# Kernel optimization log

Measured on AMD Instinct MI355X. Metric: run time of the kernel, lower is better.

The kernel has to match this reference:

```python
import jax, jax.numpy as jnp
import numpy as np

K = 3

def setup_inputs() -> dict:
    key = jax.random.key(0)
    k1, k2, k3, k4 = jax.random.split(key, 4)
    B, N, F_in, T, F_out = 8, 2048, 16, 12, 32
    x = jax.random.normal(k1, (B, N, F_in, T), dtype=jnp.float32)
    spatial_attention = jax.random.uniform(k2, (B, N, N), dtype=jnp.float32)
    node_embeddings = jax.random.normal(k3, (N, 16), dtype=jnp.float32)
    theta = jax.random.normal(k4, (K, F_in, F_out), dtype=jnp.float32) * 0.1
    return {"x": x, "spatial_attention": spatial_attention,
            "node_embeddings": node_embeddings, "theta": theta}

def _cheb_polys(node_embeddings, N, K):
    # supports = softmax(relu(E E^T), axis=1)
    supports = jax.nn.softmax(jax.nn.relu(node_embeddings @ node_embeddings.T), axis=1)
    polys = [jnp.eye(N, dtype=supports.dtype), supports]
    for _ in range(2, K):
        polys.append(2.0 * supports @ polys[-1] - polys[-2])
    return jnp.stack(polys[:K], axis=0)  # (K, N, N)

def reference(x, spatial_attention, node_embeddings, theta):
    B, N, F_in, T = x.shape
    polys = _cheb_polys(node_embeddings, N, K)             # (K,N,N)
    # T_k_with_at = polys[k] * attention (broadcast over batch);
    # rhs = T_k_with_at^T @ graph_signal for every timestep:
    # (K,N,N)*(B,N,N) contracted with (B,N,F,T) over source node n -> (K,B,M,F,T)
    rhs = jnp.einsum('knm,bnm,bnft->kbmft', polys, spatial_attention, x)
    # accumulate rhs @ theta_k over k -> (B,M,F_out,T)
    out = jnp.einsum('kbmft,kfo->bmot', rhs, theta)
    return jax.nn.relu(out)
```

## Files before the change

kernel.cpp:

```cpp
#include <hip/hip_runtime.h>

#define NN    2048
#define BATCH 8
#define FIN   16
#define TT    12
#define FOUT  32
#define FT    (FIN*TT)
#define OT    (FOUT*TT)

typedef unsigned short ushort_t;
typedef __attribute__((ext_vector_type(8))) short   short8;
typedef __attribute__((ext_vector_type(4))) float   f32x4;
typedef __attribute__((ext_vector_type(4))) unsigned short us4;
typedef __attribute__((ext_vector_type(8))) unsigned short us8;

__device__ __forceinline__ float b2f(unsigned short u) {
    union { unsigned int i; float f; } v; v.i = ((unsigned int)u) << 16; return v.f;
}
__device__ __forceinline__ unsigned short f2b(float f) {
    union { float f; unsigned int i; } v; v.f = f;
    unsigned int x = v.i;
    x += 0x7fffu + ((x >> 16) & 1u);
    return (unsigned short)(x >> 16);
}

__global__ __launch_bounds__(256)
void k_supports(const float* __restrict__ E, ushort_t* __restrict__ Sb) {
    const int n = blockIdx.x;
    __shared__ float row[NN];
    __shared__ float red[256];
    const int tid = threadIdx.x;

    float en[16];
    #pragma unroll
    for (int j = 0; j < 16; ++j) en[j] = E[n * 16 + j];

    float lmax = 0.0f;
    for (int m = tid; m < NN; m += 256) {
        float d = 0.0f;
        #pragma unroll
        for (int j = 0; j < 16; ++j) d += en[j] * E[m * 16 + j];
        d = fmaxf(d, 0.0f);
        row[m] = d;
        lmax = fmaxf(lmax, d);
    }
    red[tid] = lmax; __syncthreads();
    for (int s = 128; s > 0; s >>= 1) {
        if (tid < s) red[tid] = fmaxf(red[tid], red[tid + s]);
        __syncthreads();
    }
    const float mx = red[0];
    __syncthreads();

    float lsum = 0.0f;
    for (int m = tid; m < NN; m += 256) {
        float e = __expf(row[m] - mx);
        row[m] = e;
        lsum += e;
    }
    red[tid] = lsum; __syncthreads();
    for (int s = 128; s > 0; s >>= 1) {
        if (tid < s) red[tid] += red[tid + s];
        __syncthreads();
    }
    const float inv = 1.0f / red[0];
    for (int m = tid; m < NN; m += 256) Sb[(size_t)n * NN + m] = f2b(row[m] * inv);
}

__global__ __launch_bounds__(256)
void k_pack_st(const ushort_t* __restrict__ Sb, ushort_t* __restrict__ SbT) {
    const int r0 = blockIdx.x * 64, c0 = blockIdx.y * 64;
    __shared__ ushort_t Lt[64][65];
    const int tid = threadIdx.x;
    #pragma unroll
    for (int p = 0; p < 2; ++p) {
        const int i = (tid >> 3) + p * 32;
        const int j8 = (tid & 7) * 8;
        us8 v = *(const us8*)&Sb[(size_t)(r0 + i) * NN + c0 + j8];
        #pragma unroll
        for (int e = 0; e < 8; ++e) Lt[i][j8 + e] = v[e];
    }
    __syncthreads();
    #pragma unroll
    for (int p = 0; p < 2; ++p) {
        const int jj = (tid >> 3) + p * 32;
        const int i8 = (tid & 7) * 8;
        us8 v;
        #pragma unroll
        for (int e = 0; e < 8; ++e) v[e] = Lt[i8 + e][jj];
        *(us8*)&SbT[(size_t)(c0 + jj) * NN + r0 + i8] = v;
    }
}

__global__ __launch_bounds__(256)
void k_pack_x(const float* __restrict__ x, ushort_t* __restrict__ xbT) {
    const int nc = blockIdx.x * 64;
    const int b  = blockIdx.y;
    __shared__ ushort_t Lt[FT][65];
    const int tid = threadIdx.x;
    const float* __restrict__ xb = x + (size_t)b * NN * FT;
    #pragma unroll
    for (int p = 0; p < 12; ++p) {
        const int id = tid + 256 * p;
        const int nn = id / 48;
        const int f4 = (id % 48) * 4;
        const float4 v = *(const float4*)&xb[(size_t)(nc + nn) * FT + f4];
        Lt[f4 + 0][nn] = f2b(v.x);
        Lt[f4 + 1][nn] = f2b(v.y);
        Lt[f4 + 2][nn] = f2b(v.z);
        Lt[f4 + 3][nn] = f2b(v.w);
    }
    __syncthreads();
    #pragma unroll
    for (int p = 0; p < 6; ++p) {
        const int id = tid + 256 * p;
        const int ft = id >> 3;
        const int n8 = (id & 7) * 8;
        us8 v;
        #pragma unroll
        for (int e = 0; e < 8; ++e) v[e] = Lt[ft][n8 + e];
        *(us8*)&xbT[((size_t)b * FT + ft) * NN + nc + n8] = v;
    }
}

__global__ __launch_bounds__(256)
void k_t2(const ushort_t* __restrict__ Sb, const ushort_t* __restrict__ SbT,
          ushort_t* __restrict__ T2b) {
    const int m0 = blockIdx.x * 64;
    const int n0 = blockIdx.y * 64;
    __shared__ __align__(16) ushort_t As[2][64 * 64];
    __shared__ __align__(16) ushort_t Bs[2][64 * 64];
    const int tid = threadIdx.x;
    const int lane = tid & 63, w = tid >> 6;
    const int l15 = lane & 15, q = lane >> 4, l7 = lane & 7;
    const int n0w = (w & 1) * 32, m0w = (w >> 1) * 32;
    const int sr = tid >> 3;
    const int sc = tid & 7;

    f32x4 acc[2][2];
    #pragma unroll
    for (int i = 0; i < 2; ++i)
        #pragma unroll
        for (int j = 0; j < 2; ++j) acc[i][j] = {0.f, 0.f, 0.f, 0.f};

    us8 av[2], bv[2];
    #pragma unroll
    for (int p = 0; p < 2; ++p) {
        const int row = sr + 32 * p;
        av[p] = *(const us8*)&Sb[(size_t)(n0 + row) * NN + sc * 8];
        bv[p] = *(const us8*)&SbT[(size_t)(m0 + row) * NN + sc * 8];
    }
    #pragma unroll
    for (int p = 0; p < 2; ++p) {
        const int row = sr + 32 * p;
        const int cs = (sc ^ (row & 7)) * 8;
        *(us8*)&As[0][row * 64 + cs] = av[p];
        *(us8*)&Bs[0][row * 64 + cs] = bv[p];
    }
    for (int it = 0; it < 32; ++it) {
        __syncthreads();
        const int cur = it & 1;
        if (it < 31) {
            const int l0 = (it + 1) * 64;
            #pragma unroll
            for (int p = 0; p < 2; ++p) {
                const int row = sr + 32 * p;
                av[p] = *(const us8*)&Sb[(size_t)(n0 + row) * NN + l0 + sc * 8];
                bv[p] = *(const us8*)&SbT[(size_t)(m0 + row) * NN + l0 + sc * 8];
            }
        }
        #pragma unroll
        for (int s = 0; s < 2; ++s) {
            short8 a[2], bb[2];
            const int u = ((s * 4 + q) ^ l7) * 8;
            #pragma unroll
            for (int i = 0; i < 2; ++i)
                a[i] = *(const short8*)&As[cur][(n0w + i * 16 + l15) * 64 + u];
            #pragma unroll
            for (int j = 0; j < 2; ++j)
                bb[j] = *(const short8*)&Bs[cur][(m0w + j * 16 + l15) * 64 + u];
            #pragma unroll
            for (int i = 0; i < 2; ++i)
                #pragma unroll
                for (int j = 0; j < 2; ++j)
                    acc[i][j] = __builtin_amdgcn_mfma_f32_16x16x32_bf16(a[i], bb[j], acc[i][j], 0, 0, 0);
        }
        if (it < 31) {
            const int nxt = cur ^ 1;
            #pragma unroll
            for (int p = 0; p < 2; ++p) {
                const int row = sr + 32 * p;
                const int cs = (sc ^ (row & 7)) * 8;
                *(us8*)&As[nxt][row * 64 + cs] = av[p];
                *(us8*)&Bs[nxt][row * 64 + cs] = bv[p];
            }
        }
    }
    #pragma unroll
    for (int i = 0; i < 2; ++i)
        #pragma unroll
        for (int j = 0; j < 2; ++j)
            #pragma unroll
            for (int r = 0; r < 4; ++r) {
                const int ng = n0 + n0w + i * 16 + q * 4 + r;
                const int mg = m0 + m0w + j * 16 + l15;
                const float v = 2.0f * acc[i][j][r] - (ng == mg ? 1.0f : 0.0f);
                T2b[(size_t)ng * NN + mg] = f2b(v);
            }
}

__global__ __launch_bounds__(256)
void k_rhs(const ushort_t* __restrict__ Sb, const ushort_t* __restrict__ T2b,
           const float* __restrict__ att, const ushort_t* __restrict__ xbT,
           float* __restrict__ rhs) {
    const int m0 = blockIdx.x * 32;
    const int b  = blockIdx.y;
    __shared__ __align__(16) ushort_t As[2][2 * 32 * 64];
    __shared__ __align__(16) ushort_t Xs[2][FT * 64];
    const int tid = threadIdx.x;
    const int lane = tid & 63, w = tid >> 6;
    const int l15 = lane & 15, q = lane >> 4, l7 = lane & 7, l3 = lane >> 3;
    const int k1 = w & 1, ft0 = (w >> 1) * 96;
    const float* __restrict__ attb = att + (size_t)b * NN * NN;

    const int k1s = tid >> 7;
    const int uu  = tid & 127;
    const int m4  = (uu & 7) * 4;
    const int nn4 = (uu >> 3) * 4;
    const ushort_t* __restrict__ Pk = k1s ? T2b : Sb;

    f32x4 acc[2][6];
    #pragma unroll
    for (int i = 0; i < 2; ++i)
        #pragma unroll
        for (int t = 0; t < 6; ++t) acc[i][t] = {0.f, 0.f, 0.f, 0.f};

    us8   xv[6];
    us4   pv[4];
    f32x4 av4[4];

    #pragma unroll
    for (int p = 0; p < 6; ++p) {
        const int row = (w * 6 + p) * 8 + l3;
        xv[p] = *(const us8*)&xbT[((size_t)b * FT + row) * NN + l7 * 8];
    }
    #pragma unroll
    for (int r = 0; r < 4; ++r) {
        const int nn = nn4 + r;
        pv[r]  = *(const us4*)&Pk[(size_t)nn * NN + m0 + m4];
        av4[r] = *(const f32x4*)&attb[(size_t)nn * NN + m0 + m4];
    }
    #pragma unroll
    for (int p = 0; p < 6; ++p) {
        const int row = (w * 6 + p) * 8 + l3;
        *(us8*)&Xs[0][row * 64 + (l7 ^ l3) * 8] = xv[p];
    }
    #pragma unroll
    for (int c = 0; c < 4; ++c) {
        us4 wv;
        #pragma unroll
        for (int r = 0; r < 4; ++r) wv[r] = f2b(b2f(pv[r][c]) * av4[r][c]);
        const int rowm = m4 + c;
        const int off = (((nn4 >> 3) ^ (rowm & 7)) * 8) + (nn4 & 4);
        *(us4*)&As[0][(k1s * 32 + rowm) * 64 + off] = wv;
    }

    for (int it = 0; it < 32; ++it) {
        __syncthreads();
        const int cur = it & 1;
        if (it < 31) {
            const int nc = (it + 1) * 64;
            #pragma unroll
            for (int p = 0; p < 6; ++p) {
                const int row = (w * 6 + p) * 8 + l3;
                xv[p] = *(const us8*)&xbT[((size_t)b * FT + row) * NN + nc + l7 * 8];
            }
            #pragma unroll
            for (int r = 0; r < 4; ++r) {
                const int nn = nc + nn4 + r;
                pv[r]  = *(const us4*)&Pk[(size_t)nn * NN + m0 + m4];
                av4[r] = *(const f32x4*)&attb[(size_t)nn * NN + m0 + m4];
            }
        }
        #pragma unroll
        for (int s = 0; s < 2; ++s) {
            short8 a[2], bb[6];
            #pragma unroll
            for (int i = 0; i < 2; ++i) {
                const int row = i * 16 + l15;
                a[i] = *(const short8*)&As[cur][(k1 * 32 + row) * 64 + (((s * 4 + q) ^ l7) * 8)];
            }
            #pragma unroll
            for (int t = 0; t < 6; ++t) {
                const int col = ft0 + t * 16 + l15;
                const int u = ((s * 4 + q) ^ (col & 7)) * 8;
                bb[t] = *(const short8*)&Xs[cur][col * 64 + u];
            }
            #pragma unroll
            for (int i = 0; i < 2; ++i)
                #pragma unroll
                for (int t = 0; t < 6; ++t)
                    acc[i][t] = __builtin_amdgcn_mfma_f32_16x16x32_bf16(a[i], bb[t], acc[i][t], 0, 0, 0);
        }
        if (it < 31) {
            const int nxt = cur ^ 1;
            #pragma unroll
            for (int p = 0; p < 6; ++p) {
                const int row = (w * 6 + p) * 8 + l3;
                *(us8*)&Xs[nxt][row * 64 + (l7 ^ l3) * 8] = xv[p];
            }
            #pragma unroll
            for (int c = 0; c < 4; ++c) {
                us4 wv;
                #pragma unroll
                for (int r = 0; r < 4; ++r) wv[r] = f2b(b2f(pv[r][c]) * av4[r][c]);
                const int rowm = m4 + c;
                const int off = (((nn4 >> 3) ^ (rowm & 7)) * 8) + (nn4 & 4);
                *(us4*)&As[nxt][(k1s * 32 + rowm) * 64 + off] = wv;
            }
        }
    }
    float* __restrict__ op = rhs + ((size_t)(k1 * BATCH + b)) * NN * FT;
    #pragma unroll
    for (int i = 0; i < 2; ++i)
        #pragma unroll
        for (int t = 0; t < 6; ++t)
            #pragma unroll
            for (int r = 0; r < 4; ++r) {
                const int mg = m0 + i * 16 + q * 4 + r;
                const int ftg = ft0 + t * 16 + l15;
                op[(size_t)mg * FT + ftg] = acc[i][t][r];
            }
}

__global__ __launch_bounds__(128)
void k_out(const float* __restrict__ x, const float* __restrict__ att,
           const float* __restrict__ theta, const float* __restrict__ rhs,
           float* __restrict__ out) {
    const int m = blockIdx.x & (NN - 1);
    const int b = blockIdx.x >> 11;
    __shared__ float xr[FT], r1[FT], r2[FT];
    __shared__ float th[3 * FIN * FOUT];
    const int tid = threadIdx.x;

    const float* __restrict__ xb = x + ((size_t)b * NN + m) * FT;
    const float* __restrict__ p1 = rhs + ((size_t)0 * BATCH + b) * NN * FT + (size_t)m * FT;
    const float* __restrict__ p2 = rhs + ((size_t)1 * BATCH + b) * NN * FT + (size_t)m * FT;
    const float a0 = att[((size_t)b * NN + m) * NN + m];

    for (int i = tid; i < FT; i += 128) {
        xr[i] = xb[i] * a0;
        r1[i] = p1[i];
        r2[i] = p2[i];
    }
    for (int i = tid; i < 3 * FIN * FOUT; i += 128) th[i] = theta[i];
    __syncthreads();

    float* __restrict__ ob = out + ((size_t)b * NN + m) * OT;
    for (int idx = tid; idx < OT; idx += 128) {
        const int o = idx / TT, t = idx % TT;
        float acc = 0.0f;
        #pragma unroll
        for (int f = 0; f < FIN; ++f) {
            const int ft = f * TT + t;
            acc += th[f * FOUT + o] * xr[ft];
            acc += th[512 + f * FOUT + o] * r1[ft];
            acc += th[1024 + f * FOUT + o] * r2[ft];
        }
        ob[idx] = fmaxf(acc, 0.0f);
    }
}

extern "C" void kernel_launch(void* const* d_in, const int* in_sizes, int n_in,
                              void* d_out, int out_size, void* d_ws, size_t ws_size,
                              hipStream_t stream) {
    const float* x     = (const float*)d_in[0];
    const float* att   = (const float*)d_in[1];
    const float* E     = (const float*)d_in[2];
    const float* theta = (const float*)d_in[3];
    float* out = (float*)d_out;

    ushort_t* Sb  = (ushort_t*)d_ws;
    ushort_t* SbT = Sb  + (size_t)NN * NN;
    ushort_t* T2b = SbT + (size_t)NN * NN;
    ushort_t* xbT = T2b + (size_t)NN * NN;
    float*    rhs = (float*)(xbT + (size_t)BATCH * FT * NN);

    k_supports<<<NN, 256, 0, stream>>>(E, Sb);
    k_pack_st<<<dim3(32, 32), 256, 0, stream>>>(Sb, SbT);
    k_pack_x<<<dim3(32, BATCH), 256, 0, stream>>>(x, xbT);
    k_t2<<<dim3(32, 32), 256, 0, stream>>>(Sb, SbT, T2b);
    k_rhs<<<dim3(64, BATCH), 256, 0, stream>>>(Sb, T2b, att, xbT, rhs);
    k_out<<<BATCH * NN, 128, 0, stream>>>(x, att, theta, rhs, out);
}
```

Baseline: 336.6 us.

## Deepen global prefetch to two stages in T2 and RHS GEMMs, vectorize supports loads

```diff
diff --git a/kernel.cpp b/kernel.cpp
--- a/kernel.cpp
+++ b/kernel.cpp
@@ -31,15 +31,24 @@
     __shared__ float red[256];
     const int tid = threadIdx.x;
 
-    float en[16];
-    #pragma unroll
-    for (int j = 0; j < 16; ++j) en[j] = E[n * 16 + j];
+    const f32x4 en0 = *(const f32x4*)&E[n * 16 + 0];
+    const f32x4 en1 = *(const f32x4*)&E[n * 16 + 4];
+    const f32x4 en2 = *(const f32x4*)&E[n * 16 + 8];
+    const f32x4 en3 = *(const f32x4*)&E[n * 16 + 12];
 
     float lmax = 0.0f;
     for (int m = tid; m < NN; m += 256) {
+        const f32x4* Em = (const f32x4*)&E[(size_t)m * 16];
+        const f32x4 e0 = Em[0], e1 = Em[1], e2 = Em[2], e3 = Em[3];
         float d = 0.0f;
         #pragma unroll
-        for (int j = 0; j < 16; ++j) d += en[j] * E[m * 16 + j];
+        for (int j = 0; j < 4; ++j) d += en0[j] * e0[j];
+        #pragma unroll
+        for (int j = 0; j < 4; ++j) d += en1[j] * e1[j];
+        #pragma unroll
+        for (int j = 0; j < 4; ++j) d += en2[j] * e2[j];
+        #pragma unroll
+        for (int j = 0; j < 4; ++j) d += en3[j] * e3[j];
         d = fmaxf(d, 0.0f);
         row[m] = d;
         lmax = fmaxf(lmax, d);
@@ -123,7 +132,7 @@
     }
 }
 
-__global__ __launch_bounds__(256)
+__global__ __launch_bounds__(256, 4)
 void k_t2(const ushort_t* __restrict__ Sb, const ushort_t* __restrict__ SbT,
           ushort_t* __restrict__ T2b) {
     const int m0 = blockIdx.x * 64;
@@ -143,59 +152,54 @@
         #pragma unroll
         for (int j = 0; j < 2; ++j) acc[i][j] = {0.f, 0.f, 0.f, 0.f};
 
-    us8 av[2], bv[2];
-    #pragma unroll
-    for (int p = 0; p < 2; ++p) {
-        const int row = sr + 32 * p;
-        av[p] = *(const us8*)&Sb[(size_t)(n0 + row) * NN + sc * 8];
-        bv[p] = *(const us8*)&SbT[(size_t)(m0 + row) * NN + sc * 8];
-    }
-    #pragma unroll
-    for (int p = 0; p < 2; ++p) {
-        const int row = sr + 32 * p;
-        const int cs = (sc ^ (row & 7)) * 8;
-        *(us8*)&As[0][row * 64 + cs] = av[p];
-        *(us8*)&Bs[0][row * 64 + cs] = bv[p];
-    }
-    for (int it = 0; it < 32; ++it) {
-        __syncthreads();
-        const int cur = it & 1;
-        if (it < 31) {
-            const int l0 = (it + 1) * 64;
-            #pragma unroll
-            for (int p = 0; p < 2; ++p) {
-                const int row = sr + 32 * p;
-                av[p] = *(const us8*)&Sb[(size_t)(n0 + row) * NN + l0 + sc * 8];
-                bv[p] = *(const us8*)&SbT[(size_t)(m0 + row) * NN + l0 + sc * 8];
-            }
-        }
-        #pragma unroll
-        for (int s = 0; s < 2; ++s) {
-            short8 a[2], bb[2];
-            const int u = ((s * 4 + q) ^ l7) * 8;
-            #pragma unroll
-            for (int i = 0; i < 2; ++i)
-                a[i] = *(const short8*)&As[cur][(n0w + i * 16 + l15) * 64 + u];
-            #pragma unroll
-            for (int j = 0; j < 2; ++j)
-                bb[j] = *(const short8*)&Bs[cur][(m0w + j * 16 + l15) * 64 + u];
-            #pragma unroll
-            for (int i = 0; i < 2; ++i)
-                #pragma unroll
-                for (int j = 0; j < 2; ++j)
-                    acc[i][j] = __builtin_amdgcn_mfma_f32_16x16x32_bf16(a[i], bb[j], acc[i][j], 0, 0, 0);
-        }
-        if (it < 31) {
-            const int nxt = cur ^ 1;
-            #pragma unroll
-            for (int p = 0; p < 2; ++p) {
-                const int row = sr + 32 * p;
-                const int cs = (sc ^ (row & 7)) * 8;
-                *(us8*)&As[nxt][row * 64 + cs] = av[p];
-                *(us8*)&Bs[nxt][row * 64 + cs] = bv[p];
-            }
-        }
-    }
+    us8 avA[2], bvA[2], avB[2], bvB[2];
+
+#define T2_LOAD(l0, av, bv)                                              \
+    { _Pragma("unroll") for (int p = 0; p < 2; ++p) {                    \
+        const int row_ = sr + 32 * p;                                    \
+        av[p] = *(const us8*)&Sb[(size_t)(n0 + row_) * NN + (l0) + sc * 8];  \
+        bv[p] = *(const us8*)&SbT[(size_t)(m0 + row_) * NN + (l0) + sc * 8]; \
+      } }
+
+#define T2_STORE(bufi, av, bv)                                           \
+    { _Pragma("unroll") for (int p = 0; p < 2; ++p) {                    \
+        const int row_ = sr + 32 * p;                                    \
+        const int cs_ = (sc ^ (row_ & 7)) * 8;                           \
+        *(us8*)&As[bufi][row_ * 64 + cs_] = av[p];                       \
+        *(us8*)&Bs[bufi][row_ * 64 + cs_] = bv[p];                       \
+      } }
+
+#define T2_MFMA(bufi)                                                    \
+    { _Pragma("unroll") for (int s = 0; s < 2; ++s) {                    \
+        short8 a_[2], b_[2];                                             \
+        const int u_ = ((s * 4 + q) ^ l7) * 8;                           \
+        _Pragma("unroll") for (int i = 0; i < 2; ++i)                    \
+            a_[i] = *(const short8*)&As[bufi][(n0w + i * 16 + l15) * 64 + u_]; \
+        _Pragma("unroll") for (int j = 0; j < 2; ++j)                    \
+            b_[j] = *(const short8*)&Bs[bufi][(m0w + j * 16 + l15) * 64 + u_]; \
+        _Pragma("unroll") for (int i = 0; i < 2; ++i)                    \
+            _Pragma("unroll") for (int j = 0; j < 2; ++j)                \
+                acc[i][j] = __builtin_amdgcn_mfma_f32_16x16x32_bf16(a_[i], b_[j], acc[i][j], 0, 0, 0); \
+      } }
+
+    T2_LOAD(0, avA, bvA);
+    T2_LOAD(64, avB, bvB);
+    T2_STORE(0, avA, bvA);
+
+    for (int it = 0; it < 32; it += 2) {
+        __syncthreads();
+        if (it < 30) T2_LOAD((it + 2) * 64, avA, bvA);
+        T2_MFMA(0);
+        T2_STORE(1, avB, bvB);
+        __syncthreads();
+        if (it < 29) T2_LOAD((it + 3) * 64, avB, bvB);
+        T2_MFMA(1);
+        if (it < 30) T2_STORE(0, avA, bvA);
+    }
+#undef T2_LOAD
+#undef T2_STORE
+#undef T2_MFMA
+
     #pragma unroll
     for (int i = 0; i < 2; ++i)
         #pragma unroll
@@ -209,7 +213,7 @@
             }
 }
 
-__global__ __launch_bounds__(256)
+__global__ __launch_bounds__(256, 2)
 void k_rhs(const ushort_t* __restrict__ Sb, const ushort_t* __restrict__ T2b,
            const float* __restrict__ att, const ushort_t* __restrict__ xbT,
            float* __restrict__ rhs) {
@@ -235,91 +239,74 @@
         #pragma unroll
         for (int t = 0; t < 6; ++t) acc[i][t] = {0.f, 0.f, 0.f, 0.f};
 
-    us8   xv[6];
-    us4   pv[4];
-    f32x4 av4[4];
-
-    #pragma unroll
-    for (int p = 0; p < 6; ++p) {
-        const int row = (w * 6 + p) * 8 + l3;
-        xv[p] = *(const us8*)&xbT[((size_t)b * FT + row) * NN + l7 * 8];
-    }
-    #pragma unroll
-    for (int r = 0; r < 4; ++r) {
-        const int nn = nn4 + r;
-        pv[r]  = *(const us4*)&Pk[(size_t)nn * NN + m0 + m4];
-        av4[r] = *(const f32x4*)&attb[(size_t)nn * NN + m0 + m4];
-    }
-    #pragma unroll
-    for (int p = 0; p < 6; ++p) {
-        const int row = (w * 6 + p) * 8 + l3;
-        *(us8*)&Xs[0][row * 64 + (l7 ^ l3) * 8] = xv[p];
-    }
-    #pragma unroll
-    for (int c = 0; c < 4; ++c) {
-        us4 wv;
-        #pragma unroll
-        for (int r = 0; r < 4; ++r) wv[r] = f2b(b2f(pv[r][c]) * av4[r][c]);
-        const int rowm = m4 + c;
-        const int off = (((nn4 >> 3) ^ (rowm & 7)) * 8) + (nn4 & 4);
-        *(us4*)&As[0][(k1s * 32 + rowm) * 64 + off] = wv;
-    }
-
-    for (int it = 0; it < 32; ++it) {
-        __syncthreads();
-        const int cur = it & 1;
-        if (it < 31) {
-            const int nc = (it + 1) * 64;
-            #pragma unroll
-            for (int p = 0; p < 6; ++p) {
-                const int row = (w * 6 + p) * 8 + l3;
-                xv[p] = *(const us8*)&xbT[((size_t)b * FT + row) * NN + nc + l7 * 8];
-            }
-            #pragma unroll
-            for (int r = 0; r < 4; ++r) {
-                const int nn = nc + nn4 + r;
-                pv[r]  = *(const us4*)&Pk[(size_t)nn * NN + m0 + m4];
-                av4[r] = *(const f32x4*)&attb[(size_t)nn * NN + m0 + m4];
-            }
-        }
-        #pragma unroll
-        for (int s = 0; s < 2; ++s) {
-            short8 a[2], bb[6];
-            #pragma unroll
-            for (int i = 0; i < 2; ++i) {
-                const int row = i * 16 + l15;
-                a[i] = *(const short8*)&As[cur][(k1 * 32 + row) * 64 + (((s * 4 + q) ^ l7) * 8)];
-            }
-            #pragma unroll
-            for (int t = 0; t < 6; ++t) {
-                const int col = ft0 + t * 16 + l15;
-                const int u = ((s * 4 + q) ^ (col & 7)) * 8;
-                bb[t] = *(const short8*)&Xs[cur][col * 64 + u];
-            }
-            #pragma unroll
-            for (int i = 0; i < 2; ++i)
-                #pragma unroll
-                for (int t = 0; t < 6; ++t)
-                    acc[i][t] = __builtin_amdgcn_mfma_f32_16x16x32_bf16(a[i], bb[t], acc[i][t], 0, 0, 0);
-        }
-        if (it < 31) {
-            const int nxt = cur ^ 1;
-            #pragma unroll
-            for (int p = 0; p < 6; ++p) {
-                const int row = (w * 6 + p) * 8 + l3;
-                *(us8*)&Xs[nxt][row * 64 + (l7 ^ l3) * 8] = xv[p];
-            }
-            #pragma unroll
-            for (int c = 0; c < 4; ++c) {
-                us4 wv;
-                #pragma unroll
-                for (int r = 0; r < 4; ++r) wv[r] = f2b(b2f(pv[r][c]) * av4[r][c]);
-                const int rowm = m4 + c;
-                const int off = (((nn4 >> 3) ^ (rowm & 7)) * 8) + (nn4 & 4);
-                *(us4*)&As[nxt][(k1s * 32 + rowm) * 64 + off] = wv;
-            }
-        }
-    }
+    us8   xvA[6], xvB[6];
+    us4   pvA[4], pvB[4];
+    f32x4 avA[4], avB[4];
+
+#define RHS_LOAD(nc, xv, pv, av)                                         \
+    { _Pragma("unroll") for (int p = 0; p < 6; ++p) {                    \
+        const int row_ = (w * 6 + p) * 8 + l3;                           \
+        xv[p] = *(const us8*)&xbT[((size_t)b * FT + row_) * NN + (nc) + l7 * 8]; \
+      }                                                                  \
+      _Pragma("unroll") for (int r = 0; r < 4; ++r) {                    \
+        const int nn_ = (nc) + nn4 + r;                                  \
+        pv[r] = *(const us4*)&Pk[(size_t)nn_ * NN + m0 + m4];            \
+        av[r] = *(const f32x4*)&attb[(size_t)nn_ * NN + m0 + m4];        \
+      } }
+
+#define RHS_STORE(bufi, xv, pv, av)                                      \
+    { _Pragma("unroll") for (int p = 0; p < 6; ++p) {                    \
+        const int row_ = (w * 6 + p) * 8 + l3;                           \
+        *(us8*)&Xs[bufi][row_ * 64 + (l7 ^ l3) * 8] = xv[p];             \
+      }                                                                  \
+      _Pragma("unroll") for (int c = 0; c < 4; ++c) {                    \
+        const float w0_ = b2f(pv[0][c]) * av[0][c];                      \
+        const float w1_ = b2f(pv[1][c]) * av[1][c];                      \
+        const float w2_ = b2f(pv[2][c]) * av[2][c];                      \
+        const float w3_ = b2f(pv[3][c]) * av[3][c];                      \
+        unsigned int u01_, u23_;                                         \
+        asm("v_cvt_pk_bf16_f32 %0, %1, %2" : "=v"(u01_) : "v"(w0_), "v"(w1_)); \
+        asm("v_cvt_pk_bf16_f32 %0, %1, %2" : "=v"(u23_) : "v"(w2_), "v"(w3_)); \
+        const int rowm_ = m4 + c;                                        \
+        const int off_ = (((nn4 >> 3) ^ (rowm_ & 7)) * 8) + (nn4 & 4);   \
+        *(uint2*)&As[bufi][(k1s * 32 + rowm_) * 64 + off_] = make_uint2(u01_, u23_); \
+      } }
+
+#define RHS_MFMA(bufi)                                                   \
+    { _Pragma("unroll") for (int s = 0; s < 2; ++s) {                    \
+        short8 a_[2], bb_[6];                                            \
+        _Pragma("unroll") for (int i = 0; i < 2; ++i) {                  \
+            const int row_ = i * 16 + l15;                               \
+            a_[i] = *(const short8*)&As[bufi][(k1 * 32 + row_) * 64 + (((s * 4 + q) ^ l7) * 8)]; \
+        }                                                                \
+        _Pragma("unroll") for (int t = 0; t < 6; ++t) {                  \
+            const int col_ = ft0 + t * 16 + l15;                         \
+            const int u_ = ((s * 4 + q) ^ (col_ & 7)) * 8;               \
+            bb_[t] = *(const short8*)&Xs[bufi][col_ * 64 + u_];          \
+        }                                                                \
+        _Pragma("unroll") for (int i = 0; i < 2; ++i)                    \
+            _Pragma("unroll") for (int t = 0; t < 6; ++t)                \
+                acc[i][t] = __builtin_amdgcn_mfma_f32_16x16x32_bf16(a_[i], bb_[t], acc[i][t], 0, 0, 0); \
+      } }
+
+    RHS_LOAD(0, xvA, pvA, avA);
+    RHS_LOAD(64, xvB, pvB, avB);
+    RHS_STORE(0, xvA, pvA, avA);
+
+    for (int it = 0; it < 32; it += 2) {
+        __syncthreads();
+        if (it < 30) RHS_LOAD((it + 2) * 64, xvA, pvA, avA);
+        RHS_MFMA(0);
+        RHS_STORE(1, xvB, pvB, avB);
+        __syncthreads();
+        if (it < 29) RHS_LOAD((it + 3) * 64, xvB, pvB, avB);
+        RHS_MFMA(1);
+        if (it < 30) RHS_STORE(0, xvA, pvA, avA);
+    }
+#undef RHS_LOAD
+#undef RHS_STORE
+#undef RHS_MFMA
+
     float* __restrict__ op = rhs + ((size_t)(k1 * BATCH + b)) * NN * FT;
     #pragma unroll
     for (int i = 0; i < 2; ++i)
```

Result: no change. 338.7 us (+0.6%).
